# Kernel optimization log

Hardware: AMD Instinct MI355X
Metric: run time of the kernel (lower is better)

The kernel has to match this reference:

```python
import jax, jax.numpy as jnp
import numpy as np

# Mamba2 config derived from __init__ defaults
D_MODEL, D_STATE, D_CONV, EXPAND, HEADDIM = 768, 16, 4, 2, 64
D_INNER = EXPAND * D_MODEL                      # 1536
NHEADS = D_INNER // HEADDIM                     # 24
NGROUPS = 1
CONV_DIM = D_INNER + 2 * NGROUPS * D_STATE      # 1568
D_IN_PROJ = 2 * D_INNER + 2 * NGROUPS * D_STATE + NHEADS  # 3128
EPS = 1e-5


def setup_inputs() -> dict:
    key = jax.random.key(0)
    ks = jax.random.split(key, 8)
    B, L = 2, 4096
    x = jax.random.normal(ks[0], (B, L, D_MODEL), jnp.float32)
    s_in = 1.0 / np.sqrt(D_MODEL)
    s_out = 1.0 / np.sqrt(D_INNER)
    W_in = jax.random.uniform(ks[1], (D_IN_PROJ, D_MODEL), jnp.float32, -s_in, s_in)
    W_out = jax.random.uniform(ks[2], (D_MODEL, D_INNER), jnp.float32, -s_out, s_out)
    conv_w = jax.random.uniform(ks[3], (CONV_DIM, D_CONV), jnp.float32, -0.5, 0.5)
    conv_b = jax.random.uniform(ks[4], (CONV_DIM,), jnp.float32, -0.5, 0.5)
    # dt init in [1e-3, 0.1] (log-uniform), stored as inverse-softplus bias
    dt = jnp.exp(jax.random.uniform(ks[5], (NHEADS,), jnp.float32) * (np.log(0.1) - np.log(1e-3)) + np.log(1e-3))
    dt_bias = dt + jnp.log(-jnp.expm1(-dt))
    A_log = jnp.log(jax.random.uniform(ks[6], (NHEADS,), jnp.float32, 1.0, 16.0))
    D = jnp.ones((NHEADS,), jnp.float32)
    ln_w = jnp.ones((D_MODEL,), jnp.float32)
    ln_b = jnp.zeros((D_MODEL,), jnp.float32)
    gate_norm_w = jnp.ones((D_INNER,), jnp.float32)
    return dict(x=x, ln_w=ln_w, ln_b=ln_b, W_in=W_in, conv_w=conv_w, conv_b=conv_b,
                dt_bias=dt_bias, A_log=A_log, D=D, gate_norm_w=gate_norm_w, W_out=W_out)


def _layernorm(x, w, b):
    mu = x.mean(-1, keepdims=True)
    var = ((x - mu) ** 2).mean(-1, keepdims=True)
    return (x - mu) * jax.lax.rsqrt(var + EPS) * w + b


def _silu(x):
    return x * jax.nn.sigmoid(x)


def _mamba_block(x, ln_w, ln_b, W_in, conv_w, conv_b, dt_bias, A_log, D, gate_norm_w, W_out):
    Bsz, L, _ = x.shape
    u = _layernorm(x, ln_w, ln_b)
    zxbcdt = jnp.einsum('bld,ed->ble', u, W_in)                 # (b,l,3128)
    z = zxbcdt[..., :D_INNER]
    xBC = zxbcdt[..., D_INNER:D_INNER + CONV_DIM]
    dt = jax.nn.softplus(zxbcdt[..., -NHEADS:] + dt_bias)       # (b,l,h)
    # causal depthwise conv (width D_CONV) + SiLU
    xp = jnp.pad(xBC, ((0, 0), (D_CONV - 1, 0), (0, 0)))
    acc = xp[:, 0:L, :] * conv_w[:, 0]
    for i in range(1, D_CONV):
        acc = acc + xp[:, i:i + L, :] * conv_w[:, i]
    xBC = _silu(acc + conv_b)
    xs = xBC[..., :D_INNER].reshape(Bsz, L, NHEADS, HEADDIM)    # (b,l,h,p)
    Bm = xBC[..., D_INNER:D_INNER + D_STATE]                    # (b,l,n) ngroups=1
    Cm = xBC[..., D_INNER + D_STATE:]                           # (b,l,n)
    A = -jnp.exp(A_log)                                         # (h,)
    dA = jnp.exp(dt * A)                                        # (b,l,h)
    # selective scan: h_t = dA_t * h_{t-1} + dt_t * (x_t outer B_t)
    def step(h, inp):
        dA_t, dt_t, B_t, C_t, x_t = inp                          # (b,h),(b,h),(b,n),(b,n),(b,h,p)
        h = dA_t[..., None, None] * h + jnp.einsum('bh,bn,bhp->bhpn', dt_t, B_t, x_t)
        y = jnp.einsum('bhpn,bn->bhp', h, C_t)
        return h, y
    h0 = jnp.zeros((Bsz, NHEADS, HEADDIM, D_STATE), x.dtype)
    _, ys = jax.lax.scan(step, h0, (dA.transpose(1, 0, 2), dt.transpose(1, 0, 2),
                                    Bm.transpose(1, 0, 2), Cm.transpose(1, 0, 2),
                                    xs.transpose(1, 0, 2, 3)))
    y = ys.transpose(1, 0, 2, 3) + D[:, None] * xs               # (b,l,h,p) skip term
    y = y.reshape(Bsz, L, D_INNER)
    # gated RMSNorm: norm(y * silu(z)) * weight
    g = y * _silu(z)
    g = g * jax.lax.rsqrt((g * g).mean(-1, keepdims=True) + EPS) * gate_norm_w
    out = jnp.einsum('ble,de->bld', g, W_out)
    return x + out


def reference(x, ln_w, ln_b, W_in, conv_w, conv_b, dt_bias, A_log, D, gate_norm_w, W_out):
    return _mamba_block(x, ln_w, ln_b, W_in, conv_w, conv_b, dt_bias, A_log, D, gate_norm_w, W_out)
```

## Files before the change

kernel.cpp:

```cpp
#include <hip/hip_runtime.h>
#include <hip/hip_bf16.h>
#include <stdint.h>

#define SEQ      4096
#define BATCH    2
#define NTOK     (BATCH*SEQ)
#define DMODEL   768
#define DINNER   1536
#define NHEADS   24
#define HEADDIM  64
#define DSTATE   16
#define NPAD     3200
#define EPSV     1e-5f
#define CHUNK    64
#define NCHUNK   (SEQ/CHUNK)
#define SUB      32

typedef __bf16 bf16x8 __attribute__((ext_vector_type(8)));
typedef float  floatx4 __attribute__((ext_vector_type(4)));

__device__ __forceinline__ unsigned short f2bf(float f) {
    union { float f; uint32_t u; } v; v.f = f;
    uint32_t u = v.u;
    uint32_t r = (u + 0x7fffu + ((u >> 16) & 1u)) >> 16;
    return (unsigned short)r;
}

__device__ __forceinline__ float bf2f(unsigned short h) {
    union { uint32_t u; float f; } v; v.u = (uint32_t)h << 16;
    return v.f;
}

__device__ __forceinline__ float bfl(uint32_t u) {
    union { uint32_t u; float f; } v; v.u = u << 16; return v.f;
}
__device__ __forceinline__ float bfh(uint32_t u) {
    union { uint32_t u; float f; } v; v.u = u & 0xffff0000u; return v.f;
}
__device__ __forceinline__ uint32_t packbf(float lo, float hi) {
    return (uint32_t)f2bf(lo) | ((uint32_t)f2bf(hi) << 16);
}

__device__ __forceinline__ float siluf(float x) { return x / (1.f + __expf(-x)); }

__device__ __forceinline__ void async_cp16(const void* g, void* l) {
    __builtin_amdgcn_global_load_lds(
        (const __attribute__((address_space(1))) void*)g,
        (__attribute__((address_space(3))) void*)l,
        16, 0, 0);
}

__global__ __launch_bounds__(256) void cvt_kernel(
    const float* __restrict__ Win, const float* __restrict__ Wout,
    unsigned short* __restrict__ win16, unsigned short* __restrict__ wout16)
{
    int idx = blockIdx.x * 256 + threadIdx.x;
    const int n1 = NPAD * DMODEL;
    if (idx < n1) {
        int r = idx / DMODEL;
        win16[idx] = (r < 3128) ? f2bf(Win[idx]) : (unsigned short)0;
    } else {
        int i2 = idx - n1;
        if (i2 < DMODEL * DINNER) wout16[i2] = f2bf(Wout[i2]);
    }
}

__global__ __launch_bounds__(256) void ln_kernel(
    const float* __restrict__ x, const float* __restrict__ lnw, const float* __restrict__ lnb,
    unsigned short* __restrict__ u16)
{
    int wave = threadIdx.x >> 6, lane = threadIdx.x & 63;
    int token = blockIdx.x * 4 + wave;
    const float* row = x + (size_t)token * DMODEL;
    float4 v[3];
    float s = 0.f, ss = 0.f;
#pragma unroll
    for (int j = 0; j < 3; ++j) {
        v[j] = *(const float4*)(row + lane*4 + j*256);
        s  += v[j].x + v[j].y + v[j].z + v[j].w;
        ss += v[j].x*v[j].x + v[j].y*v[j].y + v[j].z*v[j].z + v[j].w*v[j].w;
    }
#pragma unroll
    for (int o = 32; o > 0; o >>= 1) { s += __shfl_xor(s, o, 64); ss += __shfl_xor(ss, o, 64); }
    float mean = s * (1.f/768.f);
    float var  = ss * (1.f/768.f) - mean*mean;
    float rstd = rsqrtf(var + EPSV);
    unsigned short* brow = u16 + (size_t)token * DMODEL;
#pragma unroll
    for (int j = 0; j < 3; ++j) {
        int cidx = lane*4 + j*256;
        float4 w4 = *(const float4*)(lnw + cidx);
        float4 b4 = *(const float4*)(lnb + cidx);
        float a0 = (v[j].x - mean)*rstd*w4.x + b4.x;
        float a1 = (v[j].y - mean)*rstd*w4.y + b4.y;
        float a2 = (v[j].z - mean)*rstd*w4.z + b4.z;
        float a3 = (v[j].w - mean)*rstd*w4.w + b4.w;
        ushort4 p; p.x = f2bf(a0); p.y = f2bf(a1); p.z = f2bf(a2); p.w = f2bf(a3);
        *(ushort4*)(brow + cidx) = p;
    }
}

__global__ __launch_bounds__(256) void dt_kernel(
    const float* __restrict__ raw24, const float* __restrict__ dt_bias,
    const float* __restrict__ A_log, float* __restrict__ dtT, float* __restrict__ dAT)
{
    int tid = blockIdx.x * 256 + threadIdx.x;
    int h   = tid >> 13;
    int tok = tid & (NTOK-1);
    float raw = raw24[(size_t)tok*NHEADS + h] + dt_bias[h];
    float dt = (raw > 20.f) ? raw : log1pf(__expf(raw));
    float A = -__expf(A_log[h]);
    dtT[tid] = dt;
    dAT[tid] = __expf(dt * A);
}

__global__ __launch_bounds__(256, 3) void gemm1_kernel(
    const unsigned short* __restrict__ A, const unsigned short* __restrict__ Bt,
    unsigned short* __restrict__ z16, unsigned short* __restrict__ x16,
    float* __restrict__ bcr, float* __restrict__ raw24)
{
    constexpr int K = DMODEL;
    __shared__ unsigned short As[128*64];
    __shared__ unsigned short Bs[128*64];
    const int tid  = threadIdx.x;
    const int lane = tid & 63;
    const int wave = tid >> 6;
    const int id   = blockIdx.x;
    const int xcd  = id & 7;
    const int j5   = id >> 3;
    const int m0 = (xcd*8 + (j5 & 7)) * 128;
    const int n0 = (j5 >> 3) * 128;
    const int wm = (wave & 1) * 64;
    const int wn = (wave >> 1) * 64;

    floatx4 acc[4][4];
#pragma unroll
    for (int i = 0; i < 4; ++i)
#pragma unroll
        for (int j = 0; j < 4; ++j) acc[i][j] = floatx4{0.f, 0.f, 0.f, 0.f};

    const int srow8  = lane >> 3;
    const int schunk = lane & 7;
    const int sscol  = (schunk ^ srow8) * 8;

    for (int k0 = 0; k0 < K; k0 += 64) {
        __syncthreads();
#pragma unroll
        for (int o = 0; o < 4; ++o) {
            int row = wave*32 + o*8 + srow8;
            async_cp16(A + (size_t)(m0 + row) * K + k0 + sscol, As + row*64 + schunk*8);
        }
#pragma unroll
        for (int o = 0; o < 4; ++o) {
            int row = wave*32 + o*8 + srow8;
            async_cp16(Bt + (size_t)(n0 + row) * K + k0 + sscol, Bs + row*64 + schunk*8);
        }
        __syncthreads();
        const int fr  = lane & 15;
        const int q8  = lane >> 4;
        const int key = fr & 7;
#pragma unroll
        for (int ks = 0; ks < 2; ++ks) {
            const int ch = ((ks*4 + q8) ^ key) * 8;
            bf16x8 a[4], b[4];
#pragma unroll
            for (int i = 0; i < 4; ++i)
                a[i] = *(const bf16x8*)(As + (wm + i*16 + fr)*64 + ch);
#pragma unroll
            for (int j = 0; j < 4; ++j)
                b[j] = *(const bf16x8*)(Bs + (wn + j*16 + fr)*64 + ch);
#pragma unroll
            for (int i = 0; i < 4; ++i)
#pragma unroll
                for (int j = 0; j < 4; ++j)
                    acc[i][j] = __builtin_amdgcn_mfma_f32_16x16x32_bf16(a[i], b[j], acc[i][j], 0, 0, 0);
        }
    }

    const int col = lane & 15;
    const int rq  = (lane >> 4) * 4;
    if (n0 < DINNER) {
#pragma unroll
        for (int i = 0; i < 4; ++i)
#pragma unroll
            for (int j = 0; j < 4; ++j)
#pragma unroll
                for (int r = 0; r < 4; ++r) {
                    int gm = m0 + wm + i*16 + rq + r;
                    int gn = n0 + wn + j*16 + col;
                    z16[(size_t)gm * DINNER + gn] = f2bf(acc[i][j][r]);
                }
    } else if (n0 < 3072) {
#pragma unroll
        for (int i = 0; i < 4; ++i)
#pragma unroll
            for (int j = 0; j < 4; ++j)
#pragma unroll
                for (int r = 0; r < 4; ++r) {
                    int gm = m0 + wm + i*16 + rq + r;
                    int gn = n0 + wn + j*16 + col;
                    x16[(size_t)gm * DINNER + (gn - DINNER)] = f2bf(acc[i][j][r]);
                }
    } else {
#pragma unroll
        for (int i = 0; i < 4; ++i)
#pragma unroll
            for (int j = 0; j < 4; ++j)
#pragma unroll
                for (int r = 0; r < 4; ++r) {
                    int gm = m0 + wm + i*16 + rq + r;
                    int gn = n0 + wn + j*16 + col;
                    if (gn < 3104)
                        bcr[(size_t)gm * 32 + (gn - 3072)] = acc[i][j][r];
                    else if (gn < 3128)
                        raw24[(size_t)gm * NHEADS + (gn - 3104)] = acc[i][j][r];
                }
    }
}

__global__ __launch_bounds__(256, 4) void gemm2_kernel(
    const unsigned short* __restrict__ A, const unsigned short* __restrict__ Bt,
    float* __restrict__ Cf, const float* __restrict__ resid)
{
    constexpr int K = DINNER;
    __shared__ unsigned short As[64*64];
    __shared__ unsigned short Bs[128*64];
    const int tid  = threadIdx.x;
    const int lane = tid & 63;
    const int wave = tid >> 6;
    const int id   = blockIdx.x;
    const int xcd  = id & 7;
    const int j6   = id >> 3;
    const int m0 = (xcd*16 + j6/6) * 64;
    const int n0 = (j6 % 6) * 128;
    const int wm = (wave & 1) * 32;
    const int wn = (wave >> 1) * 64;

    floatx4 acc[2][4];
#pragma unroll
    for (int i = 0; i < 2; ++i)
#pragma unroll
        for (int j = 0; j < 4; ++j) acc[i][j] = floatx4{0.f, 0.f, 0.f, 0.f};

    const int srow8  = lane >> 3;
    const int schunk = lane & 7;
    const int sscol  = (schunk ^ srow8) * 8;

    for (int k0 = 0; k0 < K; k0 += 64) {
        __syncthreads();
#pragma unroll
        for (int o = 0; o < 2; ++o) {
            int row = wave*16 + o*8 + srow8;
            async_cp16(A + (size_t)(m0 + row) * K + k0 + sscol, As + row*64 + schunk*8);
        }
#pragma unroll
        for (int o = 0; o < 4; ++o) {
            int row = wave*32 + o*8 + srow8;
            async_cp16(Bt + (size_t)(n0 + row) * K + k0 + sscol, Bs + row*64 + schunk*8);
        }
        __syncthreads();
        const int fr  = lane & 15;
        const int q8  = lane >> 4;
        const int key = fr & 7;
#pragma unroll
        for (int ks = 0; ks < 2; ++ks) {
            const int ch = ((ks*4 + q8) ^ key) * 8;
            bf16x8 a[2], b[4];
#pragma unroll
            for (int i = 0; i < 2; ++i)
                a[i] = *(const bf16x8*)(As + (wm + i*16 + fr)*64 + ch);
#pragma unroll
            for (int j = 0; j < 4; ++j)
                b[j] = *(const bf16x8*)(Bs + (wn + j*16 + fr)*64 + ch);
#pragma unroll
            for (int i = 0; i < 2; ++i)
#pragma unroll
                for (int j = 0; j < 4; ++j)
                    acc[i][j] = __builtin_amdgcn_mfma_f32_16x16x32_bf16(a[i], b[j], acc[i][j], 0, 0, 0);
        }
    }

    const int col = lane & 15;
    const int rq  = (lane >> 4) * 4;
#pragma unroll
    for (int i = 0; i < 2; ++i)
#pragma unroll
        for (int j = 0; j < 4; ++j)
#pragma unroll
            for (int r = 0; r < 4; ++r) {
                int gm = m0 + wm + i*16 + rq + r;
                int gn = n0 + wn + j*16 + col;
                Cf[(size_t)gm * DMODEL + gn] = acc[i][j][r] + resid[(size_t)gm * DMODEL + gn];
            }
}

__global__ __launch_bounds__(256) void scan_pass1(
    const unsigned short* __restrict__ x16, const float* __restrict__ bcr,
    const float* __restrict__ dAT, const float* __restrict__ dtT,
    const float* __restrict__ cw, const float* __restrict__ cb, const float* __restrict__ Dp,
    float* __restrict__ hloc, float* __restrict__ pprod, unsigned short* __restrict__ ylocal16)
{
    int wave = threadIdx.x >> 6, lane = threadIdx.x & 63;
    int blk = blockIdx.x * 4 + wave;
    int c = blk & (NCHUNK-1), bh = blk >> 6;
    int h = bh % NHEADS, b = bh / NHEADS;
    int row0 = b * SEQ + c * CHUNK;
    int l0 = c * CHUNK;
    int tb = h * NTOK + row0;
    __shared__ float bcraw[4][35][32];
    __shared__ float bcsc[4][32][32];
    __shared__ float av[4][32], dv[4][32];

    const int cx = h*64 + lane;
    float cwx0 = cw[cx*4+0], cwx1 = cw[cx*4+1], cwx2 = cw[cx*4+2], cwx3 = cw[cx*4+3];
    float cbx = cb[cx];
    const int nBC = lane & 31;
    float cwc0 = cw[(DINNER+nBC)*4+0], cwc1 = cw[(DINNER+nBC)*4+1];
    float cwc2 = cw[(DINNER+nBC)*4+2], cwc3 = cw[(DINNER+nBC)*4+3];
    float cbc = cb[DINNER+nBC];
    float Dh = Dp[h];

    float xm3 = (l0 >= 3) ? bf2f(x16[(size_t)(row0-3)*DINNER + cx]) : 0.f;
    float xm2 = (l0 >= 2) ? bf2f(x16[(size_t)(row0-2)*DINNER + cx]) : 0.f;
    float xm1 = (l0 >= 1) ? bf2f(x16[(size_t)(row0-1)*DINNER + cx]) : 0.f;

    float hst[16];
#pragma unroll
    for (int n = 0; n < 16; ++n) hst[n] = 0.f;
    float aprod = 1.f;

    for (int sc = 0; sc < CHUNK/SUB; ++sc) {
        int rb = row0 + sc * SUB;
        int lb = l0 + sc * SUB;
        __syncthreads();
#pragma unroll
        for (int it = 0; it < 5; ++it) {
            int idx = it*64 + lane;
            if (idx < 280) {
                int s = idx >> 3, q = idx & 7;
                float4 val = {0.f,0.f,0.f,0.f};
                if (lb - 3 + s >= 0)
                    val = *(const float4*)(bcr + (size_t)(rb-3+s)*32 + q*4);
                *(float4*)&bcraw[wave][s][q*4] = val;
            }
        }
        if (lane < 32) av[wave][lane] = dAT[(size_t)tb + sc*SUB + lane];
        else           dv[wave][lane-32] = dtT[(size_t)tb + sc*SUB + lane - 32];
        float xr[SUB];
#pragma unroll
        for (int s = 0; s < SUB; ++s)
            xr[s] = bf2f(x16[(size_t)(rb+s)*DINNER + cx]);
        __syncthreads();
#pragma unroll
        for (int it = 0; it < 16; ++it) {
            int s = it*2 + (lane >> 5);
            float v = cbc + bcraw[wave][s][nBC]*cwc0 + bcraw[wave][s+1][nBC]*cwc1
                          + bcraw[wave][s+2][nBC]*cwc2 + bcraw[wave][s+3][nBC]*cwc3;
            bcsc[wave][s][nBC] = siluf(v);
        }
        __syncthreads();
#pragma unroll 2
        for (int s = 0; s < SUB; ++s) {
            float a = av[wave][s];
            float xc = siluf(cbx + xm3*cwx0 + xm2*cwx1 + xm1*cwx2 + xr[s]*cwx3);
            xm3 = xm2; xm2 = xm1; xm1 = xr[s];
            float scale = dv[wave][s] * xc;
            float y = Dh * xc;
            const float4* bp4 = (const float4*)&bcsc[wave][s][0];
            float4 bv[8];
#pragma unroll
            for (int q = 0; q < 8; ++q) bv[q] = bp4[q];
            const float* bp = (const float*)bv;
#pragma unroll
            for (int n = 0; n < 16; ++n) hst[n] = a*hst[n] + scale*bp[n];
#pragma unroll
            for (int n = 0; n < 16; ++n) y += hst[n] * bp[16+n];
            aprod *= a;
            ylocal16[(size_t)(rb+s)*DINNER + cx] = f2bf(y);
        }
    }
    float* o = hloc + (size_t)blk * 1024 + lane * 16;
#pragma unroll
    for (int n = 0; n < 16; ++n) o[n] = hst[n];
    if (lane == 0) pprod[blk] = aprod;
}

__global__ __launch_bounds__(256) void scan_pass2(
    const float* __restrict__ hloc, const float* __restrict__ pprod, float* __restrict__ hstart)
{
    __shared__ float sm[64*256];
    __shared__ float pp[64];
    const int tid = threadIdx.x;
    const int bh  = blockIdx.x >> 2;
    const int q   = blockIdx.x & 3;
    const float* src = hloc + (size_t)bh * 65536 + q * 256;
#pragma unroll
    for (int it = 0; it < 16; ++it) {
        int idx = it*256 + tid;
        int c   = idx >> 6;
        int e4  = (idx & 63) * 4;
        *(float4*)&sm[c*256 + e4] = *(const float4*)(src + (size_t)c*1024 + e4);
    }
    if (tid < 64) pp[tid] = pprod[bh*64 + tid];
    __syncthreads();
    float h = 0.f;
    float* dst = hstart + (size_t)bh * 65536 + q * 256 + tid;
#pragma unroll 8
    for (int c = 0; c < 64; ++c) {
        dst[(size_t)c * 1024] = h;
        h = pp[c] * h + sm[c*256 + tid];
    }
}

__global__ __launch_bounds__(256) void scan_pass3(
    const float* __restrict__ bcr, const float* __restrict__ dAT,
    const float* __restrict__ cw, const float* __restrict__ cb,
    const float* __restrict__ hstart, unsigned short* __restrict__ ylocal16)
{
    int wave = threadIdx.x >> 6, lane = threadIdx.x & 63;
    int blk = blockIdx.x * 4 + wave;
    int c = blk & (NCHUNK-1), bh = blk >> 6;
    int h = bh % NHEADS, b = bh / NHEADS;
    int row0 = b * SEQ + c * CHUNK;
    int l0 = c * CHUNK;
    int tb = h * NTOK + row0;
    __shared__ float craw[4][35][16];
    __shared__ float csc[4][32][16];
    __shared__ float av[4][32];

    const int cx = h*64 + lane;
    const int nC = lane & 15;
    float cwc0 = cw[(DINNER+16+nC)*4+0], cwc1 = cw[(DINNER+16+nC)*4+1];
    float cwc2 = cw[(DINNER+16+nC)*4+2], cwc3 = cw[(DINNER+16+nC)*4+3];
    float cbc = cb[DINNER+16+nC];

    float h0[16];
    const float* hs = hstart + (size_t)blk * 1024 + lane * 16;
#pragma unroll
    for (int n = 0; n < 16; ++n) h0[n] = hs[n];
    float cd = 1.f;

    for (int sc = 0; sc < CHUNK/SUB; ++sc) {
        int rb = row0 + sc * SUB;
        int lb = l0 + sc * SUB;
        __syncthreads();
#pragma unroll
        for (int it = 0; it < 3; ++it) {
            int idx = it*64 + lane;
            if (idx < 140) {
                int s = idx >> 2, q = idx & 3;
                float4 val = {0.f,0.f,0.f,0.f};
                if (lb - 3 + s >= 0)
                    val = *(const float4*)(bcr + (size_t)(rb-3+s)*32 + 16 + q*4);
                *(float4*)&craw[wave][s][q*4] = val;
            }
        }
        if (lane < 32) av[wave][lane] = dAT[(size_t)tb + sc*SUB + lane];
        float yr[SUB];
#pragma unroll
        for (int s = 0; s < SUB; ++s)
            yr[s] = bf2f(ylocal16[(size_t)(rb+s)*DINNER + cx]);
        __syncthreads();
#pragma unroll
        for (int it = 0; it < 8; ++it) {
            int s = it*4 + (lane >> 4);
            float v = cbc + craw[wave][s][nC]*cwc0 + craw[wave][s+1][nC]*cwc1
                          + craw[wave][s+2][nC]*cwc2 + craw[wave][s+3][nC]*cwc3;
            csc[wave][s][nC] = siluf(v);
        }
        __syncthreads();
#pragma unroll 2
        for (int s = 0; s < SUB; ++s) {
            cd *= av[wave][s];
            const float4* cp4 = (const float4*)&csc[wave][s][0];
            float4 cv[4];
#pragma unroll
            for (int q = 0; q < 4; ++q) cv[q] = cp4[q];
            const float* cp = (const float*)cv;
            float corr = 0.f;
#pragma unroll
            for (int n = 0; n < 16; ++n) corr += cp[n] * h0[n];
            ylocal16[(size_t)(rb+s)*DINNER + cx] = f2bf(yr[s] + cd * corr);
        }
    }
}

__global__ __launch_bounds__(256) void gate_kernel(
    const unsigned short* __restrict__ yv16, const unsigned short* __restrict__ z16,
    const float* __restrict__ gw, unsigned short* __restrict__ g16)
{
    int wave = threadIdx.x >> 6, lane = threadIdx.x & 63;
    int token = blockIdx.x * 4 + wave;
    const uint4* yrow = (const uint4*)(yv16 + (size_t)token * DINNER);
    const uint4* zrow = (const uint4*)(z16 + (size_t)token * DINNER);
    float g[3][8];
    float ss = 0.f;
#pragma unroll
    for (int j = 0; j < 3; ++j) {
        uint4 y8 = yrow[lane + j*64];
        uint4 z8 = zrow[lane + j*64];
        const uint32_t* yp = (const uint32_t*)&y8;
        const uint32_t* zp = (const uint32_t*)&z8;
#pragma unroll
        for (int q = 0; q < 4; ++q) {
            float a = bfl(yp[q]) * siluf(bfl(zp[q]));
            float bvl = bfh(yp[q]) * siluf(bfh(zp[q]));
            g[j][q*2]   = a;
            g[j][q*2+1] = bvl;
            ss += a*a + bvl*bvl;
        }
    }
#pragma unroll
    for (int o = 32; o > 0; o >>= 1) ss += __shfl_xor(ss, o, 64);
    float scale = rsqrtf(ss * (1.f/1536.f) + EPSV);
    uint4* orow = (uint4*)(g16 + (size_t)token * DINNER);
#pragma unroll
    for (int j = 0; j < 3; ++j) {
        int ebase = (lane + j*64) * 8;
        float4 w0 = *(const float4*)(gw + ebase);
        float4 w1 = *(const float4*)(gw + ebase + 4);
        uint4 p;
        p.x = packbf(g[j][0]*scale*w0.x, g[j][1]*scale*w0.y);
        p.y = packbf(g[j][2]*scale*w0.z, g[j][3]*scale*w0.w);
        p.z = packbf(g[j][4]*scale*w1.x, g[j][5]*scale*w1.y);
        p.w = packbf(g[j][6]*scale*w1.z, g[j][7]*scale*w1.w);
        orow[lane + j*64] = p;
    }
}

extern "C" void kernel_launch(void* const* d_in, const int* in_sizes, int n_in,
                              void* d_out, int out_size, void* d_ws, size_t ws_size,
                              hipStream_t stream)
{
    const float* x        = (const float*)d_in[0];
    const float* ln_w     = (const float*)d_in[1];
    const float* ln_b     = (const float*)d_in[2];
    const float* W_in     = (const float*)d_in[3];
    const float* conv_w   = (const float*)d_in[4];
    const float* conv_b   = (const float*)d_in[5];
    const float* dt_bias  = (const float*)d_in[6];
    const float* A_log    = (const float*)d_in[7];
    const float* Dp       = (const float*)d_in[8];
    const float* gate_w   = (const float*)d_in[9];
    const float* W_out    = (const float*)d_in[10];
    float* out = (float*)d_out;

    char* ws = (char*)d_ws;
    size_t off = 0;
    auto alloc = [&](size_t bytes) -> void* {
        void* p = ws + off;
        off += (bytes + 255) & ~(size_t)255;
        return p;
    };
    unsigned short* u16    = (unsigned short*)alloc((size_t)NTOK*DMODEL*2);
    unsigned short* win16  = (unsigned short*)alloc((size_t)NPAD*DMODEL*2);
    float*          dtT    = (float*)alloc((size_t)NTOK*NHEADS*4);
    float*          dAT    = (float*)alloc((size_t)NTOK*NHEADS*4);
    float*          raw24  = (float*)alloc((size_t)NTOK*NHEADS*4);
    unsigned short* x16    = (unsigned short*)alloc((size_t)NTOK*DINNER*2);
    float*          bcr    = (float*)alloc((size_t)NTOK*32*4);
    unsigned short* wout16 = (unsigned short*)alloc((size_t)DMODEL*DINNER*2);
    unsigned short* z16    = (unsigned short*)alloc((size_t)NTOK*DINNER*2);
    unsigned short* y16    = (unsigned short*)alloc((size_t)NTOK*DINNER*2);
    unsigned short* g16    = (unsigned short*)alloc((size_t)NTOK*DINNER*2);
    float*          pprod  = (float*)alloc((size_t)BATCH*NHEADS*NCHUNK*4);
    float* hloc   = (float*)u16;
    float* hstart = (float*)g16;

    cvt_kernel<<<(NPAD*DMODEL + DMODEL*DINNER)/256, 256, 0, stream>>>(W_in, W_out, win16, wout16);
    ln_kernel<<<NTOK/4, 256, 0, stream>>>(x, ln_w, ln_b, u16);
    gemm1_kernel<<<1600, 256, 0, stream>>>(u16, win16, z16, x16, bcr, raw24);
    dt_kernel<<<NTOK*NHEADS/256, 256, 0, stream>>>(raw24, dt_bias, A_log, dtT, dAT);
    scan_pass1<<<BATCH*NHEADS*NCHUNK/4, 256, 0, stream>>>(x16, bcr, dAT, dtT, conv_w, conv_b, Dp, hloc, pprod, y16);
    scan_pass2<<<BATCH*NHEADS*4, 256, 0, stream>>>(hloc, pprod, hstart);
    scan_pass3<<<BATCH*NHEADS*NCHUNK/4, 256, 0, stream>>>(bcr, dAT, conv_w, conv_b, hstart, y16);
    gate_kernel<<<NTOK/4, 256, 0, stream>>>(y16, z16, gate_w, g16);
    gemm2_kernel<<<768, 256, 0, stream>>>(g16, wout16, out, x);
}
```

Measured before the change: 261.8 us.

## Fuse gate and RMSNorm into scan and GEMM epilogue; merge LN with weight conversion

Merges the layernorm and weight-conversion kernels into one launch and vectorizes the conversion. It also folds the gate norm weight into W_out. The SiLU gating moves into scan_pass3, which accumulates per-token sum-of-squares with atomics. The RMS scale is applied in the gemm2 epilogue, so gate_kernel and one full read/write of a 1536-wide bf16 activation are gone. The cost is many atomicAdds and extra per-row shuffle reductions in scan_pass3, and the RMS scale is now applied after the bf16 GEMM rather than before.

```diff
diff --git a/kernel.cpp b/kernel.cpp
--- a/kernel.cpp
+++ b/kernel.cpp
@@ -15,6 +15,7 @@
 #define CHUNK    64
 #define NCHUNK   (SEQ/CHUNK)
 #define SUB      32
+#define LNBLK    2048
 
 typedef __bf16 bf16x8 __attribute__((ext_vector_type(8)));
 typedef float  floatx4 __attribute__((ext_vector_type(4)));
@@ -50,53 +51,66 @@
         16, 0, 0);
 }
 
-__global__ __launch_bounds__(256) void cvt_kernel(
+__global__ __launch_bounds__(256) void prep_kernel(
+    const float* __restrict__ x, const float* __restrict__ lnw, const float* __restrict__ lnb,
+    unsigned short* __restrict__ u16,
     const float* __restrict__ Win, const float* __restrict__ Wout,
+    const float* __restrict__ gw,
     unsigned short* __restrict__ win16, unsigned short* __restrict__ wout16)
 {
-    int idx = blockIdx.x * 256 + threadIdx.x;
-    const int n1 = NPAD * DMODEL;
-    if (idx < n1) {
-        int r = idx / DMODEL;
-        win16[idx] = (r < 3128) ? f2bf(Win[idx]) : (unsigned short)0;
+    if (blockIdx.x < LNBLK) {
+        int wave = threadIdx.x >> 6, lane = threadIdx.x & 63;
+        int token = blockIdx.x * 4 + wave;
+        const float* row = x + (size_t)token * DMODEL;
+        float4 v[3];
+        float s = 0.f, ss = 0.f;
+#pragma unroll
+        for (int j = 0; j < 3; ++j) {
+            v[j] = *(const float4*)(row + lane*4 + j*256);
+            s  += v[j].x + v[j].y + v[j].z + v[j].w;
+            ss += v[j].x*v[j].x + v[j].y*v[j].y + v[j].z*v[j].z + v[j].w*v[j].w;
+        }
+#pragma unroll
+        for (int o = 32; o > 0; o >>= 1) { s += __shfl_xor(s, o, 64); ss += __shfl_xor(ss, o, 64); }
+        float mean = s * (1.f/768.f);
+        float var  = ss * (1.f/768.f) - mean*mean;
+        float rstd = rsqrtf(var + EPSV);
+        unsigned short* brow = u16 + (size_t)token * DMODEL;
+#pragma unroll
+        for (int j = 0; j < 3; ++j) {
+            int cidx = lane*4 + j*256;
+            float4 w4 = *(const float4*)(lnw + cidx);
+            float4 b4 = *(const float4*)(lnb + cidx);
+            float a0 = (v[j].x - mean)*rstd*w4.x + b4.x;
+            float a1 = (v[j].y - mean)*rstd*w4.y + b4.y;
+            float a2 = (v[j].z - mean)*rstd*w4.z + b4.z;
+            float a3 = (v[j].w - mean)*rstd*w4.w + b4.w;
+            ushort4 p; p.x = f2bf(a0); p.y = f2bf(a1); p.z = f2bf(a2); p.w = f2bf(a3);
+            *(ushort4*)(brow + cidx) = p;
+        }
     } else {
-        int i2 = idx - n1;
-        if (i2 < DMODEL * DINNER) wout16[i2] = f2bf(Wout[i2]);
-    }
-}
-
-__global__ __launch_bounds__(256) void ln_kernel(
-    const float* __restrict__ x, const float* __restrict__ lnw, const float* __restrict__ lnb,
-    unsigned short* __restrict__ u16)
-{
-    int wave = threadIdx.x >> 6, lane = threadIdx.x & 63;
-    int token = blockIdx.x * 4 + wave;
-    const float* row = x + (size_t)token * DMODEL;
-    float4 v[3];
-    float s = 0.f, ss = 0.f;
-#pragma unroll
-    for (int j = 0; j < 3; ++j) {
-        v[j] = *(const float4*)(row + lane*4 + j*256);
-        s  += v[j].x + v[j].y + v[j].z + v[j].w;
-        ss += v[j].x*v[j].x + v[j].y*v[j].y + v[j].z*v[j].z + v[j].w*v[j].w;
-    }
-#pragma unroll
-    for (int o = 32; o > 0; o >>= 1) { s += __shfl_xor(s, o, 64); ss += __shfl_xor(ss, o, 64); }
-    float mean = s * (1.f/768.f);
-    float var  = ss * (1.f/768.f) - mean*mean;
-    float rstd = rsqrtf(var + EPSV);
-    unsigned short* brow = u16 + (size_t)token * DMODEL;
-#pragma unroll
-    for (int j = 0; j < 3; ++j) {
-        int cidx = lane*4 + j*256;
-        float4 w4 = *(const float4*)(lnw + cidx);
-        float4 b4 = *(const float4*)(lnb + cidx);
-        float a0 = (v[j].x - mean)*rstd*w4.x + b4.x;
-        float a1 = (v[j].y - mean)*rstd*w4.y + b4.y;
-        float a2 = (v[j].z - mean)*rstd*w4.z + b4.z;
-        float a3 = (v[j].w - mean)*rstd*w4.w + b4.w;
-        ushort4 p; p.x = f2bf(a0); p.y = f2bf(a1); p.z = f2bf(a2); p.w = f2bf(a3);
-        *(ushort4*)(brow + cidx) = p;
+        int e = ((blockIdx.x - LNBLK) * 256 + threadIdx.x) * 4;
+        const int n1 = NPAD * DMODEL;
+        if (e < n1) {
+            int r = e / DMODEL;
+            ushort4 p = {0, 0, 0, 0};
+            if (r < 3128) {
+                float4 v = *(const float4*)(Win + e);
+                p.x = f2bf(v.x); p.y = f2bf(v.y); p.z = f2bf(v.z); p.w = f2bf(v.w);
+            }
+            *(ushort4*)(win16 + e) = p;
+        } else {
+            int e2 = e - n1;
+            if (e2 < DMODEL * DINNER) {
+                int row = e2 / DINNER;
+                int col = e2 - row * DINNER;
+                float4 v = *(const float4*)(Wout + e2);
+                float4 w = *(const float4*)(gw + col);
+                ushort4 p; p.x = f2bf(v.x*w.x); p.y = f2bf(v.y*w.y);
+                           p.z = f2bf(v.z*w.z); p.w = f2bf(v.w*w.w);
+                *(ushort4*)(wout16 + e2) = p;
+            }
+        }
     }
 }
 
@@ -220,7 +234,7 @@
 
 __global__ __launch_bounds__(256, 4) void gemm2_kernel(
     const unsigned short* __restrict__ A, const unsigned short* __restrict__ Bt,
-    float* __restrict__ Cf, const float* __restrict__ resid)
+    float* __restrict__ Cf, const float* __restrict__ resid, const float* __restrict__ ssb)
 {
     constexpr int K = DINNER;
     __shared__ unsigned short As[64*64];
@@ -285,13 +299,15 @@
 #pragma unroll
     for (int i = 0; i < 2; ++i)
 #pragma unroll
-        for (int j = 0; j < 4; ++j)
-#pragma unroll
-            for (int r = 0; r < 4; ++r) {
-                int gm = m0 + wm + i*16 + rq + r;
+        for (int r = 0; r < 4; ++r) {
+            int gm = m0 + wm + i*16 + rq + r;
+            float sc = rsqrtf(ssb[gm] * (1.f/1536.f) + EPSV);
+#pragma unroll
+            for (int j = 0; j < 4; ++j) {
                 int gn = n0 + wn + j*16 + col;
-                Cf[(size_t)gm * DMODEL + gn] = acc[i][j][r] + resid[(size_t)gm * DMODEL + gn];
+                Cf[(size_t)gm * DMODEL + gn] = acc[i][j][r] * sc + resid[(size_t)gm * DMODEL + gn];
             }
+        }
 }
 
 __global__ __launch_bounds__(256) void scan_pass1(
@@ -386,13 +402,16 @@
 }
 
 __global__ __launch_bounds__(256) void scan_pass2(
-    const float* __restrict__ hloc, const float* __restrict__ pprod, float* __restrict__ hstart)
+    const float* __restrict__ hloc, const float* __restrict__ pprod,
+    float* __restrict__ hstart, float* __restrict__ ssb)
 {
     __shared__ float sm[64*256];
     __shared__ float pp[64];
     const int tid = threadIdx.x;
     const int bh  = blockIdx.x >> 2;
     const int q   = blockIdx.x & 3;
+    int gt = blockIdx.x * 256 + tid;
+    if (gt < NTOK) ssb[gt] = 0.f;
     const float* src = hloc + (size_t)bh * 65536 + q * 256;
 #pragma unroll
     for (int it = 0; it < 16; ++it) {
@@ -415,7 +434,8 @@
 __global__ __launch_bounds__(256) void scan_pass3(
     const float* __restrict__ bcr, const float* __restrict__ dAT,
     const float* __restrict__ cw, const float* __restrict__ cb,
-    const float* __restrict__ hstart, unsigned short* __restrict__ ylocal16)
+    const float* __restrict__ hstart, const unsigned short* __restrict__ z16,
+    unsigned short* __restrict__ ylocal16, float* __restrict__ ssb)
 {
     int wave = threadIdx.x >> 6, lane = threadIdx.x & 63;
     int blk = blockIdx.x * 4 + wave;
@@ -456,10 +476,12 @@
             }
         }
         if (lane < 32) av[wave][lane] = dAT[(size_t)tb + sc*SUB + lane];
-        float yr[SUB];
-#pragma unroll
-        for (int s = 0; s < SUB; ++s)
+        float yr[SUB], zr[SUB];
+#pragma unroll
+        for (int s = 0; s < SUB; ++s) {
             yr[s] = bf2f(ylocal16[(size_t)(rb+s)*DINNER + cx]);
+            zr[s] = bf2f(z16[(size_t)(rb+s)*DINNER + cx]);
+        }
         __syncthreads();
 #pragma unroll
         for (int it = 0; it < 8; ++it) {
@@ -480,51 +502,13 @@
             float corr = 0.f;
 #pragma unroll
             for (int n = 0; n < 16; ++n) corr += cp[n] * h0[n];
-            ylocal16[(size_t)(rb+s)*DINNER + cx] = f2bf(yr[s] + cd * corr);
-        }
-    }
-}
-
-__global__ __launch_bounds__(256) void gate_kernel(
-    const unsigned short* __restrict__ yv16, const unsigned short* __restrict__ z16,
-    const float* __restrict__ gw, unsigned short* __restrict__ g16)
-{
-    int wave = threadIdx.x >> 6, lane = threadIdx.x & 63;
-    int token = blockIdx.x * 4 + wave;
-    const uint4* yrow = (const uint4*)(yv16 + (size_t)token * DINNER);
-    const uint4* zrow = (const uint4*)(z16 + (size_t)token * DINNER);
-    float g[3][8];
-    float ss = 0.f;
-#pragma unroll
-    for (int j = 0; j < 3; ++j) {
-        uint4 y8 = yrow[lane + j*64];
-        uint4 z8 = zrow[lane + j*64];
-        const uint32_t* yp = (const uint32_t*)&y8;
-        const uint32_t* zp = (const uint32_t*)&z8;
-#pragma unroll
-        for (int q = 0; q < 4; ++q) {
-            float a = bfl(yp[q]) * siluf(bfl(zp[q]));
-            float bvl = bfh(yp[q]) * siluf(bfh(zp[q]));
-            g[j][q*2]   = a;
-            g[j][q*2+1] = bvl;
-            ss += a*a + bvl*bvl;
-        }
-    }
-#pragma unroll
-    for (int o = 32; o > 0; o >>= 1) ss += __shfl_xor(ss, o, 64);
-    float scale = rsqrtf(ss * (1.f/1536.f) + EPSV);
-    uint4* orow = (uint4*)(g16 + (size_t)token * DINNER);
-#pragma unroll
-    for (int j = 0; j < 3; ++j) {
-        int ebase = (lane + j*64) * 8;
-        float4 w0 = *(const float4*)(gw + ebase);
-        float4 w1 = *(const float4*)(gw + ebase + 4);
-        uint4 p;
-        p.x = packbf(g[j][0]*scale*w0.x, g[j][1]*scale*w0.y);
-        p.y = packbf(g[j][2]*scale*w0.z, g[j][3]*scale*w0.w);
-        p.z = packbf(g[j][4]*scale*w1.x, g[j][5]*scale*w1.y);
-        p.w = packbf(g[j][6]*scale*w1.z, g[j][7]*scale*w1.w);
-        orow[lane + j*64] = p;
+            float g = (yr[s] + cd * corr) * siluf(zr[s]);
+            float ssp = g * g;
+#pragma unroll
+            for (int o = 32; o > 0; o >>= 1) ssp += __shfl_xor(ssp, o, 64);
+            if (lane == 0) atomicAdd(&ssb[rb + s], ssp);
+            ylocal16[(size_t)(rb+s)*DINNER + cx] = f2bf(g);
+        }
     }
 }
 
@@ -564,16 +548,16 @@
     unsigned short* y16    = (unsigned short*)alloc((size_t)NTOK*DINNER*2);
     unsigned short* g16    = (unsigned short*)alloc((size_t)NTOK*DINNER*2);
     float*          pprod  = (float*)alloc((size_t)BATCH*NHEADS*NCHUNK*4);
+    float*          ssb    = (float*)alloc((size_t)NTOK*4);
     float* hloc   = (float*)u16;
     float* hstart = (float*)g16;
 
-    cvt_kernel<<<(NPAD*DMODEL + DMODEL*DINNER)/256, 256, 0, stream>>>(W_in, W_out, win16, wout16);
-    ln_kernel<<<NTOK/4, 256, 0, stream>>>(x, ln_w, ln_b, u16);
+    prep_kernel<<<LNBLK + (NPAD*DMODEL + DMODEL*DINNER)/1024, 256, 0, stream>>>(
+        x, ln_w, ln_b, u16, W_in, W_out, gate_w, win16, wout16);
     gemm1_kernel<<<1600, 256, 0, stream>>>(u16, win16, z16, x16, bcr, raw24);
     dt_kernel<<<NTOK*NHEADS/256, 256, 0, stream>>>(raw24, dt_bias, A_log, dtT, dAT);
     scan_pass1<<<BATCH*NHEADS*NCHUNK/4, 256, 0, stream>>>(x16, bcr, dAT, dtT, conv_w, conv_b, Dp, hloc, pprod, y16);
-    scan_pass2<<<BATCH*NHEADS*4, 256, 0, stream>>>(hloc, pprod, hstart);
-    scan_pass3<<<BATCH*NHEADS*NCHUNK/4, 256, 0, stream>>>(bcr, dAT, conv_w, conv_b, hstart, y16);
-    gate_kernel<<<NTOK/4, 256, 0, stream>>>(y16, z16, gate_w, g16);
-    gemm2_kernel<<<768, 256, 0, stream>>>(g16, wout16, out, x);
-}
+    scan_pass2<<<BATCH*NHEADS*4, 256, 0, stream>>>(hloc, pprod, hstart, ssb);
+    scan_pass3<<<BATCH*NHEADS*NCHUNK/4, 256, 0, stream>>>(bcr, dAT, conv_w, conv_b, hstart, z16, y16, ssb);
+    gemm2_kernel<<<768, 256, 0, stream>>>(y16, wout16, out, x, ssb);
+}
```

Result: slower. 271.9 us (+3.9%).
